# Optimization experiments

Measured on AMD Instinct MI355X. Metric: run time of the kernel, lower is better.

## Reference

```python
import jax, jax.numpy as jnp
import numpy as np

INPUT, HIDDEN = 8, 16

def setup_inputs() -> dict:
    key = jax.random.key(0)
    ks = jax.random.split(key, 7)
    s_ih = 1.0 / np.sqrt(HIDDEN)
    x = jax.random.normal(ks[0], (8192, 512, INPUT), dtype=jnp.float32)
    W_ih = jax.random.uniform(ks[1], (HIDDEN, INPUT), jnp.float32, -s_ih, s_ih)
    W_hh = jax.random.uniform(ks[2], (HIDDEN, HIDDEN), jnp.float32, -s_ih, s_ih)
    b_ih = jax.random.uniform(ks[3], (HIDDEN,), jnp.float32, -s_ih, s_ih)
    b_hh = jax.random.uniform(ks[4], (HIDDEN,), jnp.float32, -s_ih, s_ih)
    s_fc = 1.0 / np.sqrt(HIDDEN)
    fc_w = jax.random.uniform(ks[5], (1, HIDDEN), jnp.float32, -s_fc, s_fc)
    fc_b = jax.random.uniform(ks[6], (1,), jnp.float32, -s_fc, s_fc)
    return {"x": x, "W_ih": W_ih, "W_hh": W_hh, "b_ih": b_ih, "b_hh": b_hh, "fc_w": fc_w, "fc_b": fc_b}

def reference(x, W_ih, W_hh, b_ih, b_hh, fc_w, fc_b):
    B, T, _ = x.shape
    # Precompute input projection for all timesteps: [B, T, H]
    xp = jnp.einsum('bti,hi->bth', x, W_ih) + b_ih + b_hh
    h0 = jnp.zeros((B, HIDDEN), dtype=x.dtype)

    def step(h, xt):
        h_new = jnp.tanh(xt + h @ W_hh.T)
        return h_new, None

    h_last, _ = jax.lax.scan(step, h0, jnp.swapaxes(xp, 0, 1))
    return h_last @ fc_w.T + fc_b  # [B, 1]
```

## Files before the change

### kernel.cpp

```cpp
#include <hip/hip_runtime.h>
#include <stdint.h>


#define RNN_B   8192
#define RNN_T   512
#define RNN_IN  8
#define RNN_H   16
#define TC      32
#define NE      16
#define XROW    260
#define NTILE   (RNN_T / TC)
#define BUFSZ   (NE * XROW)

typedef __fp16 half8  __attribute__((ext_vector_type(8)));
typedef __fp16 half2v __attribute__((ext_vector_type(2)));
typedef float  f32x4  __attribute__((ext_vector_type(4)));

union H8U { half8 v; __fp16 e[8]; uint32_t u[4]; };
union H2U { half2v h; uint32_t u; };

static __device__ __forceinline__ uint32_t pkh(float a, float b) {
    H2U t; t.h = __builtin_amdgcn_cvt_pkrtz(a, b); return t.u;
}
static __device__ __forceinline__ uint32_t bp32(int addr, uint32_t v) {
    return (uint32_t)__builtin_amdgcn_ds_bpermute(addr, (int)v);
}

static __device__ __forceinline__ void stage(const float* __restrict__ x,
                                             float* lds_base, int b0, int t0,
                                             int lane)
{
#pragma unroll
    for (int e = 0; e < NE; ++e) {
        const float* gp = x + ((size_t)(b0 + e) * RNN_T + t0) * RNN_IN + lane * 4;
        float* lp = lds_base + e * XROW;
        __builtin_amdgcn_global_load_lds(
            (const __attribute__((address_space(1))) uint32_t*)gp,
            (__attribute__((address_space(3))) uint32_t*)lp,
            16, 0, 0);
    }
}

__global__ __launch_bounds__(64) void rnn_mfma_kernel(
    const float* __restrict__ x,
    const float* __restrict__ W_ih,
    const float* __restrict__ W_hh,
    const float* __restrict__ b_ih,
    const float* __restrict__ b_hh,
    const float* __restrict__ fc_w,
    const float* __restrict__ fc_b,
    float* __restrict__ out)
{
    __shared__ __align__(16) float xs[2 * BUFSZ];

    const int lane = (int)threadIdx.x;
    const int col  = lane & 15;
    const int q    = lane >> 4;
    const int b0   = (int)blockIdx.x * NE;
    const bool hi32  = (lane & 32) != 0;
    const int addr32 = (lane ^ 32) << 2;
    const float C2 = 2.8853900817779268f;

    H8U A1, A2;
#pragma unroll
    for (int j = 0; j < 8; ++j) {
        const int i = j >> 1, hb = j & 1;
        const int u = 4 * ((i < 2) ? q : (q ^ 2)) + 2 * (i & 1) + hb;
        const float v = -2.0f * C2 * W_hh[col * RNN_H + u];
        const __fp16 vh = (__fp16)v;
        A1.e[j] = vh;
        if (q < 2) A2.e[j] = (__fp16)(v - (float)vh);
    }
    if (q >= 2) {
#pragma unroll
        for (int j = 0; j < 8; ++j) {
            const float uu = C2 * W_ih[col * RNN_IN + j];
            const __fp16 uh = (__fp16)uu;
            A2.e[j] = (q == 2) ? uh : (__fp16)(uu - (float)uh);
        }
    }

    f32x4 cb;
#pragma unroll
    for (int rr = 0; rr < 4; ++rr) {
        const int u = 4 * q + rr;
        float s = 0.0f;
        for (int k = 0; k < RNN_H; ++k) {
            const float v = -2.0f * C2 * W_hh[u * RNN_H + k];
            const __fp16 vh = (__fp16)v;
            const __fp16 vl = (__fp16)(v - (float)vh);
            s += (float)vh + (float)vl;
        }
        cb[rr] = C2 * (b_ih[u] + b_hh[u]) - 0.5f * s;
    }

    stage(x, xs, b0, 0, lane);
    __syncthreads();

    uint32_t rh0 = pkh(0.5f, 0.5f), rh1 = pkh(0.5f, 0.5f);
    uint32_t rl0 = 0u, rl1 = 0u;

    for (int tile = 0; tile < NTILE; ++tile) {
        const int cur = tile & 1;
        if (tile + 1 < NTILE)
            stage(x, xs + (cur ^ 1) * BUFSZ, b0, (tile + 1) * TC, lane);

        const float* xg = xs + cur * BUFSZ + col * XROW;

#pragma unroll 4
        for (int tt = 0; tt < TC; ++tt) {
            const float4 xa = *(const float4*)(xg + tt * 8);
            const float4 xb = *(const float4*)(xg + tt * 8 + 4);
            const uint32_t xh0 = pkh(xa.x, xa.y), xh1 = pkh(xa.z, xa.w);
            const uint32_t xh2 = pkh(xb.x, xb.y), xh3 = pkh(xb.z, xb.w);

            const uint32_t G0h = bp32(addr32, rh0), G1h = bp32(addr32, rh1);
            const uint32_t G0l = bp32(addr32, rl0), G1l = bp32(addr32, rl1);

            H8U B1, B2;
            B1.u[0] = hi32 ? rl0 : rh0;  B1.u[1] = hi32 ? rl1 : rh1;
            B1.u[2] = hi32 ? G0l : G0h;  B1.u[3] = hi32 ? G1l : G1h;
            B2.u[0] = hi32 ? xh0 : rh0;  B2.u[1] = hi32 ? xh1 : rh1;
            B2.u[2] = hi32 ? xh2 : G0h;  B2.u[3] = hi32 ? xh3 : G1h;

            f32x4 acc = __builtin_amdgcn_mfma_f32_16x16x32_f16(A1.v, B1.v, cb, 0, 0, 0);
            acc = __builtin_amdgcn_mfma_f32_16x16x32_f16(A2.v, B2.v, acc, 0, 0, 0);

            const float r0 = __builtin_amdgcn_rcpf(__builtin_amdgcn_exp2f(acc[0]) + 1.0f);
            const float r1 = __builtin_amdgcn_rcpf(__builtin_amdgcn_exp2f(acc[1]) + 1.0f);
            const float r2 = __builtin_amdgcn_rcpf(__builtin_amdgcn_exp2f(acc[2]) + 1.0f);
            const float r3 = __builtin_amdgcn_rcpf(__builtin_amdgcn_exp2f(acc[3]) + 1.0f);

            rh0 = pkh(r0, r1); rh1 = pkh(r2, r3);
            H2U u0, u1; u0.u = rh0; u1.u = rh1;
            rl0 = pkh(r0 - (float)u0.h[0], r1 - (float)u0.h[1]);
            rl1 = pkh(r2 - (float)u1.h[0], r3 - (float)u1.h[1]);
        }
        __syncthreads();
    }

    H2U a0, a1, c0, c1;
    a0.u = rh0; a1.u = rh1; c0.u = rl0; c1.u = rl1;
    const float h0 = 1.0f - 2.0f * ((float)a0.h[0] + (float)c0.h[0]);
    const float h1 = 1.0f - 2.0f * ((float)a0.h[1] + (float)c0.h[1]);
    const float h2 = 1.0f - 2.0f * ((float)a1.h[0] + (float)c1.h[0]);
    const float h3 = 1.0f - 2.0f * ((float)a1.h[1] + (float)c1.h[1]);
    float p = fc_w[4 * q + 0] * h0 + fc_w[4 * q + 1] * h1
            + fc_w[4 * q + 2] * h2 + fc_w[4 * q + 3] * h3;
    p += __shfl_xor(p, 16);
    p += __shfl_xor(p, 32);
    if (lane < 16) out[b0 + col] = p + fc_b[0];
}

extern "C" void kernel_launch(void* const* d_in, const int* in_sizes, int n_in,
                              void* d_out, int out_size, void* d_ws, size_t ws_size,
                              hipStream_t stream)
{
    const float* x    = (const float*)d_in[0];
    const float* W_ih = (const float*)d_in[1];
    const float* W_hh = (const float*)d_in[2];
    const float* b_ih = (const float*)d_in[3];
    const float* b_hh = (const float*)d_in[4];
    const float* fc_w = (const float*)d_in[5];
    const float* fc_b = (const float*)d_in[6];
    float* out = (float*)d_out;

    dim3 grid(RNN_B / NE);
    dim3 block(64);
    rnn_mfma_kernel<<<grid, block, 0, stream>>>(x, W_ih, W_hh, b_ih, b_hh, fc_w, fc_b, out);
}
```

Baseline: 266.6 us.

## Remove bpermute exchange by re-splitting MFMA K layout and running MFMAs independently

Reorganizes the K-dimension layout of the two MFMA operands so that each lane's quadrant supplies its own hidden-state halves and a slice of the input. This removes the four ds_bpermute cross-lane exchanges and lane-dependent selects that sat on the recurrent critical path. The two MFMAs now accumulate independently (the second from zero) and are summed before the exp, which breaks the serial MFMA dependency at the cost of four extra adds. Each lane now loads only a float2 of x per step, and the inner loop unroll goes from 4 to 8.

Result: faster. 233.8 us (-12.3%).

```diff
diff --git a/kernel.cpp b/kernel.cpp
--- a/kernel.cpp
+++ b/kernel.cpp
@@ -21,9 +21,6 @@
 
 static __device__ __forceinline__ uint32_t pkh(float a, float b) {
     H2U t; t.h = __builtin_amdgcn_cvt_pkrtz(a, b); return t.u;
-}
-static __device__ __forceinline__ uint32_t bp32(int addr, uint32_t v) {
-    return (uint32_t)__builtin_amdgcn_ds_bpermute(addr, (int)v);
 }
 
 static __device__ __forceinline__ void stage(const float* __restrict__ x,
@@ -57,27 +54,26 @@
     const int col  = lane & 15;
     const int q    = lane >> 4;
     const int b0   = (int)blockIdx.x * NE;
-    const bool hi32  = (lane & 32) != 0;
-    const int addr32 = (lane ^ 32) << 2;
     const float C2 = 2.8853900817779268f;
 
     H8U A1, A2;
 #pragma unroll
-    for (int j = 0; j < 8; ++j) {
-        const int i = j >> 1, hb = j & 1;
-        const int u = 4 * ((i < 2) ? q : (q ^ 2)) + 2 * (i & 1) + hb;
+    for (int j = 0; j < 4; ++j) {
+        const int u = 4 * q + j;
         const float v = -2.0f * C2 * W_hh[col * RNN_H + u];
         const __fp16 vh = (__fp16)v;
-        A1.e[j] = vh;
-        if (q < 2) A2.e[j] = (__fp16)(v - (float)vh);
+        const __fp16 vl = (__fp16)(v - (float)vh);
+        A1.e[j]     = vh;
+        A1.e[j + 4] = vl;
+        A2.e[j]     = vh;
     }
-    if (q >= 2) {
 #pragma unroll
-        for (int j = 0; j < 8; ++j) {
-            const float uu = C2 * W_ih[col * RNN_IN + j];
-            const __fp16 uh = (__fp16)uu;
-            A2.e[j] = (q == 2) ? uh : (__fp16)(uu - (float)uh);
-        }
+    for (int j = 0; j < 2; ++j) {
+        const int f = 2 * q + j;
+        const float uu = C2 * W_ih[col * RNN_IN + f];
+        const __fp16 uh = (__fp16)uu;
+        A2.e[4 + j] = uh;
+        A2.e[6 + j] = (__fp16)(uu - (float)uh);
     }
 
     f32x4 cb;
@@ -93,6 +89,7 @@
         }
         cb[rr] = C2 * (b_ih[u] + b_hh[u]) - 0.5f * s;
     }
+    const f32x4 zero4 = {0.0f, 0.0f, 0.0f, 0.0f};
 
     stage(x, xs, b0, 0, lane);
     __syncthreads();
@@ -105,31 +102,24 @@
         if (tile + 1 < NTILE)
             stage(x, xs + (cur ^ 1) * BUFSZ, b0, (tile + 1) * TC, lane);
 
-        const float* xg = xs + cur * BUFSZ + col * XROW;
+        const float* xg = xs + cur * BUFSZ + col * XROW + 2 * q;
 
-#pragma unroll 4
+#pragma unroll 8
         for (int tt = 0; tt < TC; ++tt) {
-            const float4 xa = *(const float4*)(xg + tt * 8);
-            const float4 xb = *(const float4*)(xg + tt * 8 + 4);
-            const uint32_t xh0 = pkh(xa.x, xa.y), xh1 = pkh(xa.z, xa.w);
-            const uint32_t xh2 = pkh(xb.x, xb.y), xh3 = pkh(xb.z, xb.w);
-
-            const uint32_t G0h = bp32(addr32, rh0), G1h = bp32(addr32, rh1);
-            const uint32_t G0l = bp32(addr32, rl0), G1l = bp32(addr32, rl1);
+            const float2 xf = *(const float2*)(xg + tt * 8);
+            const uint32_t xq = pkh(xf.x, xf.y);
 
             H8U B1, B2;
-            B1.u[0] = hi32 ? rl0 : rh0;  B1.u[1] = hi32 ? rl1 : rh1;
-            B1.u[2] = hi32 ? G0l : G0h;  B1.u[3] = hi32 ? G1l : G1h;
-            B2.u[0] = hi32 ? xh0 : rh0;  B2.u[1] = hi32 ? xh1 : rh1;
-            B2.u[2] = hi32 ? xh2 : G0h;  B2.u[3] = hi32 ? xh3 : G1h;
+            B1.u[0] = rh0; B1.u[1] = rh1; B1.u[2] = rh0; B1.u[3] = rh1;
+            B2.u[0] = rl0; B2.u[1] = rl1; B2.u[2] = xq;  B2.u[3] = xq;
 
-            f32x4 acc = __builtin_amdgcn_mfma_f32_16x16x32_f16(A1.v, B1.v, cb, 0, 0, 0);
-            acc = __builtin_amdgcn_mfma_f32_16x16x32_f16(A2.v, B2.v, acc, 0, 0, 0);
+            const f32x4 ac1 = __builtin_amdgcn_mfma_f32_16x16x32_f16(A1.v, B1.v, cb,    0, 0, 0);
+            const f32x4 ac2 = __builtin_amdgcn_mfma_f32_16x16x32_f16(A2.v, B2.v, zero4, 0, 0, 0);
 
-            const float r0 = __builtin_amdgcn_rcpf(__builtin_amdgcn_exp2f(acc[0]) + 1.0f);
-            const float r1 = __builtin_amdgcn_rcpf(__builtin_amdgcn_exp2f(acc[1]) + 1.0f);
-            const float r2 = __builtin_amdgcn_rcpf(__builtin_amdgcn_exp2f(acc[2]) + 1.0f);
-            const float r3 = __builtin_amdgcn_rcpf(__builtin_amdgcn_exp2f(acc[3]) + 1.0f);
+            const float r0 = __builtin_amdgcn_rcpf(__builtin_amdgcn_exp2f(ac1[0] + ac2[0]) + 1.0f);
+            const float r1 = __builtin_amdgcn_rcpf(__builtin_amdgcn_exp2f(ac1[1] + ac2[1]) + 1.0f);
+            const float r2 = __builtin_amdgcn_rcpf(__builtin_amdgcn_exp2f(ac1[2] + ac2[2]) + 1.0f);
+            const float r3 = __builtin_amdgcn_rcpf(__builtin_amdgcn_exp2f(ac1[3] + ac2[3]) + 1.0f);
 
             rh0 = pkh(r0, r1); rh1 = pkh(r2, r3);
             H2U u0, u1; u0.u = rh0; u1.u = rh1;
```
